# Optimization experiments

Measured on AMD Instinct MI355X. Metric: run time of the kernel, lower is better.

## Reference

```python
import math
import jax, jax.numpy as jnp
import numpy as np

B, T, C = 2, 2048, 1024
H, HKV, HD = 16, 4, 64  # n_head, n_kv_head, head_dim
G = H // HKV            # GQA groups
WS = 1024               # sliding window size
GATE_CH = 32


def setup_inputs() -> dict:
    key = jax.random.key(0)
    ks = jax.random.split(key, 8)
    x = jax.random.normal(ks[0], (B, T, C), dtype=jnp.float32)
    ve = jax.random.normal(ks[1], (B, T, HKV * HD), dtype=jnp.float32)
    # realistic RoPE tables: half head_dim frequencies
    d = HD // 2
    inv_freq = 1.0 / (10000.0 ** (jnp.arange(d, dtype=jnp.float32) / d))
    angles = jnp.arange(T, dtype=jnp.float32)[:, None] * inv_freq[None, :]  # (T, d)
    cos = jnp.cos(angles)[None, :, None, :]  # (1, T, 1, d)
    sin = jnp.sin(angles)[None, :, None, :]
    s = 0.02
    Wq = s * jax.random.normal(ks[2], (C, H * HD), dtype=jnp.float32)
    Wk = s * jax.random.normal(ks[3], (C, HKV * HD), dtype=jnp.float32)
    Wv = s * jax.random.normal(ks[4], (C, HKV * HD), dtype=jnp.float32)
    Wproj = s * jax.random.normal(ks[5], (C, C), dtype=jnp.float32)
    Wg = s * jax.random.normal(ks[6], (GATE_CH, HKV), dtype=jnp.float32)
    return {"x": x, "ve": ve, "cos": cos, "sin": sin,
            "Wq": Wq, "Wk": Wk, "Wv": Wv, "Wproj": Wproj, "Wg": Wg, "ws": WS}


def _rope(u, cos, sin):
    d = u.shape[-1] // 2
    u1, u2 = u[..., :d], u[..., d:]
    return jnp.concatenate([u1 * cos + u2 * sin, -u1 * sin + u2 * cos], axis=-1)


def _rmsnorm(u):
    eps = jnp.finfo(u.dtype).eps
    return u * jax.lax.rsqrt(jnp.mean(u * u, axis=-1, keepdims=True) + eps)


def reference(x, ve, cos, sin, Wq, Wk, Wv, Wproj, Wg, ws):
    b, t, c = x.shape
    q = (x @ Wq).reshape(b, t, H, HD)
    k = (x @ Wk).reshape(b, t, HKV, HD)
    v = (x @ Wv).reshape(b, t, HKV, HD)
    # value-embedding gate: 2*sigmoid over first 32 channels of x
    gate = 2.0 * jax.nn.sigmoid(x[..., :GATE_CH] @ Wg)  # (b, t, HKV)
    v = v + gate[..., None] * ve.reshape(b, t, HKV, HD)
    q = _rmsnorm(_rope(q, cos, sin))
    k = _rmsnorm(_rope(k, cos, sin))
    # GQA: view q as (b, t, HKV, G, HD), contract against shared k/v per kv-head
    qg = q.reshape(b, t, HKV, G, HD)
    scale = 1.0 / math.sqrt(HD)
    scores = jnp.einsum('bqhgd,bkhd->bhgqk', qg, k) * scale  # (b, HKV, G, t, t)
    pos = jnp.arange(t)
    # key j attends iff i - ws + 1 <= j <= i (sliding causal window)
    mask = (pos[None, :] >= pos[:, None] - ws + 1) & (pos[None, :] <= pos[:, None])
    scores = jnp.where(mask[None, None, None], scores, -jnp.inf)
    attn = jax.nn.softmax(scores, axis=-1)
    y = jnp.einsum('bhgqk,bkhd->bqhgd', attn, v).reshape(b, t, H * HD)
    return y @ Wproj
```

## Files before the change

### kernel.cpp

```cpp
#include <hip/hip_runtime.h>
#include <hip/hip_bf16.h>

#define Bq 2
#define Tq 2048
#define Cq 1024
#define Hq 16
#define HKVq 4
#define HDq 64
#define Gq 4
#define WSq 1024
#define GATE_CHq 32

typedef __attribute__((ext_vector_type(8))) short short8;
typedef __attribute__((ext_vector_type(4))) float f32x4;
typedef __attribute__((ext_vector_type(16))) float f32x16;
typedef __attribute__((ext_vector_type(2))) unsigned int u32x2;
typedef unsigned int u32;
typedef unsigned short u16;

#if __has_builtin(__builtin_amdgcn_exp2f)
#define EXP2(x) __builtin_amdgcn_exp2f(x)
#else
#define EXP2(x) exp2f(x)
#endif

__device__ __forceinline__ u16 f2bf(float f) {
  u32 u = __float_as_uint(f);
  u32 r = (u + 0x7FFFu + ((u >> 16) & 1u)) >> 16;
  return (u16)r;
}
__device__ __forceinline__ float bf2f(u16 u) {
  return __uint_as_float(((u32)u) << 16);
}

__device__ __forceinline__ void gl_lds16(const u16* g, u16* l) {
  __builtin_amdgcn_global_load_lds(
      (const u32 __attribute__((address_space(1)))*)g,
      (u32 __attribute__((address_space(3)))*)l, 16, 0, 0);
}

__global__ __launch_bounds__(256) void qkv_gemm_fused(
    const u16* __restrict__ A, const u16* __restrict__ Bt,
    const float* __restrict__ ve, const float* __restrict__ cosp,
    const float* __restrict__ sinp, const float* __restrict__ gatebuf,
    u16* __restrict__ Qb, u16* __restrict__ Kb, u16* __restrict__ Vtb) {
  __shared__ __attribute__((aligned(16))) u16 As[64 * 64];
  __shared__ __attribute__((aligned(16))) u16 Bs[128 * 64];

  const int bx = blockIdx.x;
  const int bm0 = blockIdx.y * 64, bn0 = bx * 128;
  const int tid = threadIdx.x;
  const int w = tid >> 6, lane = tid & 63;
  const int wm = (w >> 1) * 32, wn = (w & 1) * 64;
  const int quad = lane >> 4, l16 = lane & 15;
  const int K = 1024;

  f32x4 acc[2][4];
#pragma unroll
  for (int mt = 0; mt < 2; mt++)
#pragma unroll
    for (int nt = 0; nt < 4; nt++) acc[mt][nt] = (f32x4){0.f, 0.f, 0.f, 0.f};

  int goffA[2], goffB[4];
#pragma unroll
  for (int i = 0; i < 2; i++) {
    int s = i * 256 + tid;
    int m = s >> 3, gp = s & 7;
    goffA[i] = m * K + (gp ^ (m & 7)) * 8;
  }
#pragma unroll
  for (int i = 0; i < 4; i++) {
    int s = i * 256 + tid;
    int m = s >> 3, gp = s & 7;
    goffB[i] = m * K + (gp ^ (m & 7)) * 8;
  }
  const u16* Ab = A + (long)bm0 * K;
  const u16* Bb = Bt + (long)bn0 * K;

  for (int k0 = 0; k0 < K; k0 += 64) {
    __syncthreads();
#pragma unroll
    for (int i = 0; i < 2; i++)
      gl_lds16(Ab + goffA[i] + k0, &As[(i * 256 + w * 64) * 8]);
#pragma unroll
    for (int i = 0; i < 4; i++)
      gl_lds16(Bb + goffB[i] + k0, &Bs[(i * 256 + w * 64) * 8]);
    __syncthreads();

#pragma unroll
    for (int ks = 0; ks < 2; ks++) {
      short8 af[2], bf[4];
#pragma unroll
      for (int mt = 0; mt < 2; mt++) {
        int ml = wm + mt * 16 + l16;
        af[mt] = *(const short8*)&As[ml * 64 + (((ks * 4 + quad) ^ (ml & 7)) * 8)];
      }
#pragma unroll
      for (int nt = 0; nt < 4; nt++) {
        int nl = wn + nt * 16 + l16;
        bf[nt] = *(const short8*)&Bs[nl * 64 + (((ks * 4 + quad) ^ (nl & 7)) * 8)];
      }
#pragma unroll
      for (int mt = 0; mt < 2; mt++)
#pragma unroll
        for (int nt = 0; nt < 4; nt++)
          acc[mt][nt] = __builtin_amdgcn_mfma_f32_16x16x32_bf16(
              af[mt], bf[nt], acc[mt][nt], 0, 0, 0);
    }
  }

  const int b = bm0 >> 11;
  const int tseq0 = (bm0 & 2047) + wm;

  if (bx < 10) {
    u16* Dst;
    if (bx < 8) {
      int hh = bx * 2 + (w & 1);
      int hkv = hh >> 2, g = hh & 3;
      Dst = Qb + ((long)((b * 4 + hkv) * 4 + g) * Tq) * 64;
    } else {
      int kk = (bx - 8) * 2 + (w & 1);
      Dst = Kb + ((long)(b * 4 + kk) * Tq) * 64;
    }
#pragma unroll
    for (int mt = 0; mt < 2; mt++) {
#pragma unroll
      for (int r = 0; r < 4; r++) {
        int t = tseq0 + mt * 16 + quad * 4 + r;
        float c0 = cosp[t * 32 + l16];
        float s0 = sinp[t * 32 + l16];
        float c1 = cosp[t * 32 + 16 + l16];
        float s1 = sinp[t * 32 + 16 + l16];
        float a0 = acc[mt][0][r], a1 = acc[mt][1][r];
        float a2 = acc[mt][2][r], a3 = acc[mt][3][r];
        float rp0 = a0 * c0 + a2 * s0;
        float rp1 = a1 * c1 + a3 * s1;
        float rp2 = a2 * c0 - a0 * s0;
        float rp3 = a3 * c1 - a1 * s1;
        float ss = rp0 * rp0 + rp1 * rp1 + rp2 * rp2 + rp3 * rp3;
        ss += __shfl_xor(ss, 1);
        ss += __shfl_xor(ss, 2);
        ss += __shfl_xor(ss, 4);
        ss += __shfl_xor(ss, 8);
        float sc = rsqrtf(ss * (1.f / 64.f) + 1.1920928955078125e-07f);
        u16* drow = Dst + (long)t * 64;
        drow[l16] = f2bf(rp0 * sc);
        drow[16 + l16] = f2bf(rp1 * sc);
        drow[32 + l16] = f2bf(rp2 * sc);
        drow[48 + l16] = f2bf(rp3 * sc);
      }
    }
  } else {
    int kk = (bx - 10) * 2 + (w & 1);
    u16* Dst = Vtb + ((long)(b * 4 + kk) * 64) * Tq;
#pragma unroll
    for (int mt = 0; mt < 2; mt++) {
      float vals[4][4];
#pragma unroll
      for (int r = 0; r < 4; r++) {
        int t = tseq0 + mt * 16 + quad * 4 + r;
        long bt = (long)b * Tq + t;
        float gv = gatebuf[bt * 4 + kk];
        const float* verow = ve + bt * 256 + kk * 64;
#pragma unroll
        for (int nt = 0; nt < 4; nt++)
          vals[nt][r] = acc[mt][nt][r] + gv * verow[nt * 16 + l16];
      }
      int t0m = tseq0 + mt * 16 + quad * 4;
#pragma unroll
      for (int nt = 0; nt < 4; nt++) {
        int d = nt * 16 + l16;
        union { short4 v; u16 u[4]; } p;
#pragma unroll
        for (int r = 0; r < 4; r++) p.u[r] = f2bf(vals[nt][r]);
        *(short4*)(Dst + (long)d * Tq + t0m) = p.v;
      }
    }
  }
}

__global__ __launch_bounds__(256) void gemm_proj(
    const u16* __restrict__ A, const u16* __restrict__ Bt,
    float* __restrict__ C, int M, int N, int K) {
  __shared__ __attribute__((aligned(16))) u16 As[64 * 64];
  __shared__ __attribute__((aligned(16))) u16 Bs[128 * 64];

  const int bm0 = blockIdx.y * 64, bn0 = blockIdx.x * 128;
  const int tid = threadIdx.x;
  const int w = tid >> 6, lane = tid & 63;
  const int wm = (w >> 1) * 32, wn = (w & 1) * 64;
  const int quad = lane >> 4, l16 = lane & 15;

  f32x4 acc[2][4];
#pragma unroll
  for (int mt = 0; mt < 2; mt++)
#pragma unroll
    for (int nt = 0; nt < 4; nt++) acc[mt][nt] = (f32x4){0.f, 0.f, 0.f, 0.f};

  int goffA[2], goffB[4];
#pragma unroll
  for (int i = 0; i < 2; i++) {
    int s = i * 256 + tid;
    int m = s >> 3, gp = s & 7;
    goffA[i] = m * K + (gp ^ (m & 7)) * 8;
  }
#pragma unroll
  for (int i = 0; i < 4; i++) {
    int s = i * 256 + tid;
    int m = s >> 3, gp = s & 7;
    goffB[i] = m * K + (gp ^ (m & 7)) * 8;
  }
  const u16* Ab = A + (long)bm0 * K;
  const u16* Bb = Bt + (long)bn0 * K;

  for (int k0 = 0; k0 < K; k0 += 64) {
    __syncthreads();
#pragma unroll
    for (int i = 0; i < 2; i++)
      gl_lds16(Ab + goffA[i] + k0, &As[(i * 256 + w * 64) * 8]);
#pragma unroll
    for (int i = 0; i < 4; i++)
      gl_lds16(Bb + goffB[i] + k0, &Bs[(i * 256 + w * 64) * 8]);
    __syncthreads();

#pragma unroll
    for (int ks = 0; ks < 2; ks++) {
      short8 af[2], bf[4];
#pragma unroll
      for (int mt = 0; mt < 2; mt++) {
        int ml = wm + mt * 16 + l16;
        af[mt] = *(const short8*)&As[ml * 64 + (((ks * 4 + quad) ^ (ml & 7)) * 8)];
      }
#pragma unroll
      for (int nt = 0; nt < 4; nt++) {
        int nl = wn + nt * 16 + l16;
        bf[nt] = *(const short8*)&Bs[nl * 64 + (((ks * 4 + quad) ^ (nl & 7)) * 8)];
      }
#pragma unroll
      for (int mt = 0; mt < 2; mt++)
#pragma unroll
        for (int nt = 0; nt < 4; nt++)
          acc[mt][nt] = __builtin_amdgcn_mfma_f32_16x16x32_bf16(
              af[mt], bf[nt], acc[mt][nt], 0, 0, 0);
    }
  }

#pragma unroll
  for (int mt = 0; mt < 2; mt++)
#pragma unroll
    for (int nt = 0; nt < 4; nt++) {
      int row0 = bm0 + wm + mt * 16 + quad * 4;
      int col = bn0 + wn + nt * 16 + l16;
#pragma unroll
      for (int r = 0; r < 4; r++)
        C[(long)(row0 + r) * N + col] = acc[mt][nt][r];
    }
}

__global__ __launch_bounds__(256) void prep(
    const float* __restrict__ x, u16* __restrict__ xb,
    const float* __restrict__ Wq, const float* __restrict__ Wk,
    const float* __restrict__ Wv, const float* __restrict__ Wproj,
    const float* __restrict__ Wg, u16* __restrict__ Dqkv,
    u16* __restrict__ Dproj, float* __restrict__ gatebuf) {
  __shared__ float tile[64][65];
  int bx = blockIdx.x;
  int tid = threadIdx.x;
  if (bx < 2048) {
    int i = (bx * 256 + tid) * 8;
    float4 a = *(const float4*)(x + i);
    float4 b = *(const float4*)(x + i + 4);
    union { short8 v; u16 u[8]; } o;
    o.u[0] = f2bf(a.x); o.u[1] = f2bf(a.y); o.u[2] = f2bf(a.z); o.u[3] = f2bf(a.w);
    o.u[4] = f2bf(b.x); o.u[5] = f2bf(b.y); o.u[6] = f2bf(b.z); o.u[7] = f2bf(b.w);
    *(short8*)(xb + i) = o.v;
    return;
  }
  if (bx >= 2688) {
    int p = (bx - 2688) * 256 + tid;
    int bt = p >> 2, kk = p & 3;
    const float* xr = x + (long)bt * Cq;
    float dot = 0.f;
#pragma unroll
    for (int i = 0; i < GATE_CHq; i++) dot += xr[i] * Wg[i * HKVq + kk];
    gatebuf[p] = 2.f / (1.f + expf(-dot));
    return;
  }
  int wb = bx - 2048;
  int obx = wb >> 4;
  int k0 = (wb & 15) * 64;
  const float* S;
  u16* Dst;
  int N, nb;
  if (obx < 16)      { S = Wq;    N = 1024; nb = obx;      Dst = Dqkv; }
  else if (obx < 20) { S = Wk;    N = 256;  nb = obx - 16; Dst = Dqkv + 1024 * 1024; }
  else if (obx < 24) { S = Wv;    N = 256;  nb = obx - 20; Dst = Dqkv + 1280 * 1024; }
  else               { S = Wproj; N = 1024; nb = obx - 24; Dst = Dproj; }
  int n0 = nb * 64;
#pragma unroll
  for (int i = 0; i < 16; i++) {
    int idx = i * 256 + tid;
    int kl = idx >> 6, nl = idx & 63;
    tile[kl][nl] = S[(long)(k0 + kl) * N + n0 + nl];
  }
  __syncthreads();
#pragma unroll
  for (int i = 0; i < 16; i++) {
    int idx = i * 256 + tid;
    int nl = idx >> 6, kl = idx & 63;
    Dst[(long)(n0 + nl) * 1024 + k0 + kl] = f2bf(tile[kl][nl]);
  }
}

#define CEXP 0.18033688011112042f
#define CEXP8 1.4426950408889634f

template <bool MASK>
__device__ __forceinline__ void attn_tile32(
    int k0, int q0, int l31, int hl, const u16* __restrict__ Ks,
    const u16* __restrict__ Vts, const short8 (&QB)[4], f32x16& O0, f32x16& O1,
    float& lsum) {
  const int qpos = q0 + l31;
#pragma unroll
  for (int c = 0; c < 4; c++) {
    const int key = c * 32 + l31;
    f32x16 S;
#pragma unroll
    for (int i = 0; i < 16; i++) S[i] = 0.f;
#pragma unroll
    for (int s = 0; s < 4; s++) {
      short8 kf = *(const short8*)&Ks[key * 64 + (((s * 2 + hl) ^ (key & 7)) * 8)];
      S = __builtin_amdgcn_mfma_f32_32x32x16_bf16(kf, QB[s], S, 0, 0, 0);
    }
    const int kb = k0 + c * 32 + 4 * hl;
    float p[16];
#pragma unroll
    for (int r = 0; r < 16; r++) {
      float sv = S[r];
      if (MASK) {
        int kpos = kb + (r & 3) + 8 * (r >> 2);
        u32 diff = (u32)(qpos - kpos);
        sv = (diff < (u32)WSq) ? sv : -1e30f;
      }
      float pv = EXP2(__builtin_fmaf(sv, CEXP, -CEXP8));
      lsum += pv;
      p[r] = pv;
    }
    u32 w[8];
#pragma unroll
    for (int i = 0; i < 8; i++) {
      u32 lo = __float_as_uint(p[2 * i]) + 0x8000u;
      u32 hi = __float_as_uint(p[2 * i + 1]) + 0x8000u;
      w[i] = __builtin_amdgcn_perm(hi, lo, 0x07060302u);
    }
    u32x2 r02 = __builtin_amdgcn_permlane32_swap(w[0], w[2], false, false);
    u32x2 r13 = __builtin_amdgcn_permlane32_swap(w[1], w[3], false, false);
    u32x2 r46 = __builtin_amdgcn_permlane32_swap(w[4], w[6], false, false);
    u32x2 r57 = __builtin_amdgcn_permlane32_swap(w[5], w[7], false, false);
    union { short8 s8; u32 u[4]; } f0, f1;
    f0.u[0] = r02[0]; f0.u[1] = r13[0]; f0.u[2] = r02[1]; f0.u[3] = r13[1];
    f1.u[0] = r46[0]; f1.u[1] = r57[0]; f1.u[2] = r46[1]; f1.u[3] = r57[1];
    const int d0 = l31, d1 = 32 + l31;
    const int sw = (l31 & 7);
#pragma unroll
    for (int kc = 0; kc < 2; kc++) {
      int grp = c * 4 + kc * 2 + hl;
      short8 v0 = *(const short8*)&Vts[d0 * 128 + ((grp ^ sw) * 8)];
      short8 v1 = *(const short8*)&Vts[d1 * 128 + ((grp ^ sw) * 8)];
      const short8 pf = kc ? f1.s8 : f0.s8;
      O0 = __builtin_amdgcn_mfma_f32_32x32x16_bf16(v0, pf, O0, 0, 0, 0);
      O1 = __builtin_amdgcn_mfma_f32_32x32x16_bf16(v1, pf, O1, 0, 0, 0);
    }
  }
}

__global__ __launch_bounds__(256, 2) void attn_mfma(
    const u16* __restrict__ Qb, const u16* __restrict__ Kb,
    const u16* __restrict__ Vtb, u16* __restrict__ Yb) {
  __shared__ __attribute__((aligned(16))) u16 Ks[2][128 * 64];
  __shared__ __attribute__((aligned(16))) u16 Vts[2][64 * 128];

  int bid = blockIdx.x;
  int bh = bid & 7;
  int qt32 = bid >> 3;
  int hkv = bh & 3;
  int b = bh >> 2;
  int q0 = qt32 * 32;
  int tid = threadIdx.x;
  int g = tid >> 6;
  int lane = tid & 63;
  int l31 = lane & 31;
  int hl = lane >> 5;

  short8 QB[4];
  {
    const u16* qb =
        Qb + ((long)((bh * 4 + g) * Tq + q0 + l31)) * 64 + hl * 8;
#pragma unroll
    for (int s = 0; s < 4; s++) QB[s] = *(const short8*)(qb + s * 16);
  }

  f32x16 O0, O1;
#pragma unroll
  for (int i = 0; i < 16; i++) { O0[i] = 0.f; O1[i] = 0.f; }
  float lsum = 0.f;

  int lo = q0 - (WSq - 1);
  int st = (lo < 0 ? 0 : lo) >> 7;
  int et = (q0 + 31) >> 7;

  const u16* Kbase = Kb + ((long)bh * Tq) * 64;
  const u16* Vbase = Vtb + ((long)bh * 64) * Tq;

  int rowoffK[4], rowoffV[4];
#pragma unroll
  for (int i = 0; i < 4; i++) {
    int s = i * 256 + tid;
    int kr = s >> 3, kgp = s & 7;
    rowoffK[i] = kr * 64 + (kgp ^ (kr & 7)) * 8;
    int d = s >> 4, vgp = s & 15;
    rowoffV[i] = d * Tq + (vgp ^ (d & 7)) * 8;
  }

  {
    int k0 = st << 7;
#pragma unroll
    for (int i = 0; i < 4; i++) {
      gl_lds16(Kbase + (long)k0 * 64 + rowoffK[i], &Ks[0][(i * 256 + g * 64) * 8]);
      gl_lds16(Vbase + k0 + rowoffV[i], &Vts[0][(i * 256 + g * 64) * 8]);
    }
  }
  __syncthreads();

  int cur = 0;
  for (int kt = st; kt <= et; kt++) {
    int k0 = kt << 7;
    if (kt < et) {
      int k0n = k0 + 128;
#pragma unroll
      for (int i = 0; i < 4; i++) {
        gl_lds16(Kbase + (long)k0n * 64 + rowoffK[i],
                 &Ks[cur ^ 1][(i * 256 + g * 64) * 8]);
        gl_lds16(Vbase + k0n + rowoffV[i],
                 &Vts[cur ^ 1][(i * 256 + g * 64) * 8]);
      }
    }
    bool needC = (k0 + 127 > q0);
    bool needW = (k0 < q0 - 992);
    if (needC || needW) {
      attn_tile32<true>(k0, q0, l31, hl, Ks[cur], Vts[cur], QB, O0, O1, lsum);
    } else {
      attn_tile32<false>(k0, q0, l31, hl, Ks[cur], Vts[cur], QB, O0, O1, lsum);
    }
    __syncthreads();
    cur ^= 1;
  }

  lsum += __shfl_xor(lsum, 32);
  float invl = 1.f / lsum;

  int h = hkv * 4 + g;
  u16* yrow = Yb + ((long)(b * Tq + q0 + l31)) * 1024 + h * 64;
#pragma unroll
  for (int g4 = 0; g4 < 4; g4++) {
    union { short4 v; u16 u[4]; } pk0, pk1;
#pragma unroll
    for (int i = 0; i < 4; i++) {
      pk0.u[i] = f2bf(O0[g4 * 4 + i] * invl);
      pk1.u[i] = f2bf(O1[g4 * 4 + i] * invl);
    }
    int dA = 8 * g4 + 4 * hl;
    *(short4*)(yrow + dA) = pk0.v;
    *(short4*)(yrow + 32 + dA) = pk1.v;
  }
}

extern "C" void kernel_launch(void* const* d_in, const int* in_sizes, int n_in,
                              void* d_out, int out_size, void* d_ws,
                              size_t ws_size, hipStream_t stream) {
  const float* x     = (const float*)d_in[0];
  const float* ve    = (const float*)d_in[1];
  const float* cosp  = (const float*)d_in[2];
  const float* sinp  = (const float*)d_in[3];
  const float* Wq    = (const float*)d_in[4];
  const float* Wk    = (const float*)d_in[5];
  const float* Wv    = (const float*)d_in[6];
  const float* Wproj = (const float*)d_in[7];
  const float* Wg    = (const float*)d_in[8];

  char* base = (char*)d_ws;
  u16* xb      = (u16*)(base);
  u16* Yb      = xb;
  u16* WqkvT   = (u16*)(base + 8388608);
  u16* WprojT  = (u16*)(base + 11534336);
  u16* Qb      = (u16*)(base + 13631488);
  u16* Kb      = (u16*)(base + 22020096);
  u16* Vtb     = (u16*)(base + 24117248);
  float* gateb = (float*)(base + 26214400);
  float* out = (float*)d_out;

  prep<<<2752, 256, 0, stream>>>(x, xb, Wq, Wk, Wv, Wproj, Wg, WqkvT, WprojT,
                                 gateb);
  qkv_gemm_fused<<<dim3(12, 64), 256, 0, stream>>>(xb, WqkvT, ve, cosp, sinp,
                                                   gateb, Qb, Kb, Vtb);
  attn_mfma<<<512, 256, 0, stream>>>(Qb, Kb, Vtb, Yb);
  gemm_proj<<<dim3(8, 64), 256, 0, stream>>>(Yb, WprojT, out, 4096, 1024, 1024);
}
```

Baseline: 162.7 us.

## Enlarge GEMM tiles to 128x128 and add MFMA priority hints in attention

Both the QKV and projection GEMMs now use 128x128 block tiles, with each wave computing a 64x64 sub-tile, so operand reuse per LDS load goes up and the grid halves. The attention inner loop wraps its MFMA sections in s_setprio and splits the softmax row-sum into two accumulators to shorten the dependency chain. The larger tiles raise register and LDS use and leave fewer blocks (384 and 256) to spread across the CUs.

Result: slower. 172.9 us (+6.2%).

```diff
diff --git a/kernel.cpp b/kernel.cpp
--- a/kernel.cpp
+++ b/kernel.cpp
@@ -29,9 +29,6 @@
   u32 r = (u + 0x7FFFu + ((u >> 16) & 1u)) >> 16;
   return (u16)r;
 }
-__device__ __forceinline__ float bf2f(u16 u) {
-  return __uint_as_float(((u32)u) << 16);
-}
 
 __device__ __forceinline__ void gl_lds16(const u16* g, u16* l) {
   __builtin_amdgcn_global_load_lds(
@@ -44,35 +41,29 @@
     const float* __restrict__ ve, const float* __restrict__ cosp,
     const float* __restrict__ sinp, const float* __restrict__ gatebuf,
     u16* __restrict__ Qb, u16* __restrict__ Kb, u16* __restrict__ Vtb) {
-  __shared__ __attribute__((aligned(16))) u16 As[64 * 64];
+  __shared__ __attribute__((aligned(16))) u16 As[128 * 64];
   __shared__ __attribute__((aligned(16))) u16 Bs[128 * 64];
 
   const int bx = blockIdx.x;
-  const int bm0 = blockIdx.y * 64, bn0 = bx * 128;
+  const int bm0 = blockIdx.y * 128, bn0 = bx * 128;
   const int tid = threadIdx.x;
   const int w = tid >> 6, lane = tid & 63;
-  const int wm = (w >> 1) * 32, wn = (w & 1) * 64;
+  const int wm = (w >> 1) * 64, wn = (w & 1) * 64;
   const int quad = lane >> 4, l16 = lane & 15;
   const int K = 1024;
 
-  f32x4 acc[2][4];
-#pragma unroll
-  for (int mt = 0; mt < 2; mt++)
+  f32x4 acc[4][4];
+#pragma unroll
+  for (int mt = 0; mt < 4; mt++)
 #pragma unroll
     for (int nt = 0; nt < 4; nt++) acc[mt][nt] = (f32x4){0.f, 0.f, 0.f, 0.f};
 
-  int goffA[2], goffB[4];
-#pragma unroll
-  for (int i = 0; i < 2; i++) {
-    int s = i * 256 + tid;
-    int m = s >> 3, gp = s & 7;
-    goffA[i] = m * K + (gp ^ (m & 7)) * 8;
-  }
+  int goff[4];
 #pragma unroll
   for (int i = 0; i < 4; i++) {
     int s = i * 256 + tid;
     int m = s >> 3, gp = s & 7;
-    goffB[i] = m * K + (gp ^ (m & 7)) * 8;
+    goff[i] = m * K + (gp ^ (m & 7)) * 8;
   }
   const u16* Ab = A + (long)bm0 * K;
   const u16* Bb = Bt + (long)bn0 * K;
@@ -80,18 +71,17 @@
   for (int k0 = 0; k0 < K; k0 += 64) {
     __syncthreads();
 #pragma unroll
-    for (int i = 0; i < 2; i++)
-      gl_lds16(Ab + goffA[i] + k0, &As[(i * 256 + w * 64) * 8]);
-#pragma unroll
-    for (int i = 0; i < 4; i++)
-      gl_lds16(Bb + goffB[i] + k0, &Bs[(i * 256 + w * 64) * 8]);
+    for (int i = 0; i < 4; i++) {
+      gl_lds16(Ab + goff[i] + k0, &As[(i * 256 + w * 64) * 8]);
+      gl_lds16(Bb + goff[i] + k0, &Bs[(i * 256 + w * 64) * 8]);
+    }
     __syncthreads();
 
 #pragma unroll
     for (int ks = 0; ks < 2; ks++) {
-      short8 af[2], bf[4];
-#pragma unroll
-      for (int mt = 0; mt < 2; mt++) {
+      short8 af[4], bf[4];
+#pragma unroll
+      for (int mt = 0; mt < 4; mt++) {
         int ml = wm + mt * 16 + l16;
         af[mt] = *(const short8*)&As[ml * 64 + (((ks * 4 + quad) ^ (ml & 7)) * 8)];
       }
@@ -101,7 +91,7 @@
         bf[nt] = *(const short8*)&Bs[nl * 64 + (((ks * 4 + quad) ^ (nl & 7)) * 8)];
       }
 #pragma unroll
-      for (int mt = 0; mt < 2; mt++)
+      for (int mt = 0; mt < 4; mt++)
 #pragma unroll
         for (int nt = 0; nt < 4; nt++)
           acc[mt][nt] = __builtin_amdgcn_mfma_f32_16x16x32_bf16(
@@ -123,7 +113,7 @@
       Dst = Kb + ((long)(b * 4 + kk) * Tq) * 64;
     }
 #pragma unroll
-    for (int mt = 0; mt < 2; mt++) {
+    for (int mt = 0; mt < 4; mt++) {
 #pragma unroll
       for (int r = 0; r < 4; r++) {
         int t = tseq0 + mt * 16 + quad * 4 + r;
@@ -154,7 +144,7 @@
     int kk = (bx - 10) * 2 + (w & 1);
     u16* Dst = Vtb + ((long)(b * 4 + kk) * 64) * Tq;
 #pragma unroll
-    for (int mt = 0; mt < 2; mt++) {
+    for (int mt = 0; mt < 4; mt++) {
       float vals[4][4];
 #pragma unroll
       for (int r = 0; r < 4; r++) {
@@ -170,10 +160,10 @@
 #pragma unroll
       for (int nt = 0; nt < 4; nt++) {
         int d = nt * 16 + l16;
-        union { short4 v; u16 u[4]; } p;
-#pragma unroll
-        for (int r = 0; r < 4; r++) p.u[r] = f2bf(vals[nt][r]);
-        *(short4*)(Dst + (long)d * Tq + t0m) = p.v;
+        union { short4 v; u16 u[4]; } pk;
+#pragma unroll
+        for (int r = 0; r < 4; r++) pk.u[r] = f2bf(vals[nt][r]);
+        *(short4*)(Dst + (long)d * Tq + t0m) = pk.v;
       }
     }
   }
@@ -182,33 +172,27 @@
 __global__ __launch_bounds__(256) void gemm_proj(
     const u16* __restrict__ A, const u16* __restrict__ Bt,
     float* __restrict__ C, int M, int N, int K) {
-  __shared__ __attribute__((aligned(16))) u16 As[64 * 64];
+  __shared__ __attribute__((aligned(16))) u16 As[128 * 64];
   __shared__ __attribute__((aligned(16))) u16 Bs[128 * 64];
 
-  const int bm0 = blockIdx.y * 64, bn0 = blockIdx.x * 128;
+  const int bm0 = blockIdx.y * 128, bn0 = blockIdx.x * 128;
   const int tid = threadIdx.x;
   const int w = tid >> 6, lane = tid & 63;
-  const int wm = (w >> 1) * 32, wn = (w & 1) * 64;
+  const int wm = (w >> 1) * 64, wn = (w & 1) * 64;
   const int quad = lane >> 4, l16 = lane & 15;
 
-  f32x4 acc[2][4];
-#pragma unroll
-  for (int mt = 0; mt < 2; mt++)
+  f32x4 acc[4][4];
+#pragma unroll
+  for (int mt = 0; mt < 4; mt++)
 #pragma unroll
     for (int nt = 0; nt < 4; nt++) acc[mt][nt] = (f32x4){0.f, 0.f, 0.f, 0.f};
 
-  int goffA[2], goffB[4];
-#pragma unroll
-  for (int i = 0; i < 2; i++) {
-    int s = i * 256 + tid;
-    int m = s >> 3, gp = s & 7;
-    goffA[i] = m * K + (gp ^ (m & 7)) * 8;
-  }
+  int goff[4];
 #pragma unroll
   for (int i = 0; i < 4; i++) {
     int s = i * 256 + tid;
     int m = s >> 3, gp = s & 7;
-    goffB[i] = m * K + (gp ^ (m & 7)) * 8;
+    goff[i] = m * K + (gp ^ (m & 7)) * 8;
   }
   const u16* Ab = A + (long)bm0 * K;
   const u16* Bb = Bt + (long)bn0 * K;
@@ -216,18 +200,17 @@
   for (int k0 = 0; k0 < K; k0 += 64) {
     __syncthreads();
 #pragma unroll
-    for (int i = 0; i < 2; i++)
-      gl_lds16(Ab + goffA[i] + k0, &As[(i * 256 + w * 64) * 8]);
-#pragma unroll
-    for (int i = 0; i < 4; i++)
-      gl_lds16(Bb + goffB[i] + k0, &Bs[(i * 256 + w * 64) * 8]);
+    for (int i = 0; i < 4; i++) {
+      gl_lds16(Ab + goff[i] + k0, &As[(i * 256 + w * 64) * 8]);
+      gl_lds16(Bb + goff[i] + k0, &Bs[(i * 256 + w * 64) * 8]);
+    }
     __syncthreads();
 
 #pragma unroll
     for (int ks = 0; ks < 2; ks++) {
-      short8 af[2], bf[4];
-#pragma unroll
-      for (int mt = 0; mt < 2; mt++) {
+      short8 af[4], bf[4];
+#pragma unroll
+      for (int mt = 0; mt < 4; mt++) {
         int ml = wm + mt * 16 + l16;
         af[mt] = *(const short8*)&As[ml * 64 + (((ks * 4 + quad) ^ (ml & 7)) * 8)];
       }
@@ -237,7 +220,7 @@
         bf[nt] = *(const short8*)&Bs[nl * 64 + (((ks * 4 + quad) ^ (nl & 7)) * 8)];
       }
 #pragma unroll
-      for (int mt = 0; mt < 2; mt++)
+      for (int mt = 0; mt < 4; mt++)
 #pragma unroll
         for (int nt = 0; nt < 4; nt++)
           acc[mt][nt] = __builtin_amdgcn_mfma_f32_16x16x32_bf16(
@@ -246,7 +229,7 @@
   }
 
 #pragma unroll
-  for (int mt = 0; mt < 2; mt++)
+  for (int mt = 0; mt < 4; mt++)
 #pragma unroll
     for (int nt = 0; nt < 4; nt++) {
       int row0 = bm0 + wm + mt * 16 + quad * 4;
@@ -327,13 +310,16 @@
     f32x16 S;
 #pragma unroll
     for (int i = 0; i < 16; i++) S[i] = 0.f;
+    __builtin_amdgcn_s_setprio(1);
 #pragma unroll
     for (int s = 0; s < 4; s++) {
       short8 kf = *(const short8*)&Ks[key * 64 + (((s * 2 + hl) ^ (key & 7)) * 8)];
       S = __builtin_amdgcn_mfma_f32_32x32x16_bf16(kf, QB[s], S, 0, 0, 0);
     }
+    __builtin_amdgcn_s_setprio(0);
     const int kb = k0 + c * 32 + 4 * hl;
     float p[16];
+    float la0 = 0.f, la1 = 0.f;
 #pragma unroll
     for (int r = 0; r < 16; r++) {
       float sv = S[r];
@@ -343,25 +329,27 @@
         sv = (diff < (u32)WSq) ? sv : -1e30f;
       }
       float pv = EXP2(__builtin_fmaf(sv, CEXP, -CEXP8));
-      lsum += pv;
+      if (r & 1) la1 += pv; else la0 += pv;
       p[r] = pv;
     }
-    u32 w[8];
+    lsum += la0 + la1;
+    u32 w8[8];
 #pragma unroll
     for (int i = 0; i < 8; i++) {
       u32 lo = __float_as_uint(p[2 * i]) + 0x8000u;
       u32 hi = __float_as_uint(p[2 * i + 1]) + 0x8000u;
-      w[i] = __builtin_amdgcn_perm(hi, lo, 0x07060302u);
-    }
-    u32x2 r02 = __builtin_amdgcn_permlane32_swap(w[0], w[2], false, false);
-    u32x2 r13 = __builtin_amdgcn_permlane32_swap(w[1], w[3], false, false);
-    u32x2 r46 = __builtin_amdgcn_permlane32_swap(w[4], w[6], false, false);
-    u32x2 r57 = __builtin_amdgcn_permlane32_swap(w[5], w[7], false, false);
+      w8[i] = __builtin_amdgcn_perm(hi, lo, 0x07060302u);
+    }
+    u32x2 r02 = __builtin_amdgcn_permlane32_swap(w8[0], w8[2], false, false);
+    u32x2 r13 = __builtin_amdgcn_permlane32_swap(w8[1], w8[3], false, false);
+    u32x2 r46 = __builtin_amdgcn_permlane32_swap(w8[4], w8[6], false, false);
+    u32x2 r57 = __builtin_amdgcn_permlane32_swap(w8[5], w8[7], false, false);
     union { short8 s8; u32 u[4]; } f0, f1;
     f0.u[0] = r02[0]; f0.u[1] = r13[0]; f0.u[2] = r02[1]; f0.u[3] = r13[1];
     f1.u[0] = r46[0]; f1.u[1] = r57[0]; f1.u[2] = r46[1]; f1.u[3] = r57[1];
     const int d0 = l31, d1 = 32 + l31;
     const int sw = (l31 & 7);
+    __builtin_amdgcn_s_setprio(1);
 #pragma unroll
     for (int kc = 0; kc < 2; kc++) {
       int grp = c * 4 + kc * 2 + hl;
@@ -371,6 +359,7 @@
       O0 = __builtin_amdgcn_mfma_f32_32x32x16_bf16(v0, pf, O0, 0, 0, 0);
       O1 = __builtin_amdgcn_mfma_f32_32x32x16_bf16(v1, pf, O1, 0, 0, 0);
     }
+    __builtin_amdgcn_s_setprio(0);
   }
 }
 
@@ -497,12 +486,12 @@
   u16* Kb      = (u16*)(base + 22020096);
   u16* Vtb     = (u16*)(base + 24117248);
   float* gateb = (float*)(base + 26214400);
-  float* out = (float*)d_out;
+  float* out   = (float*)d_out;
 
   prep<<<2752, 256, 0, stream>>>(x, xb, Wq, Wk, Wv, Wproj, Wg, WqkvT, WprojT,
                                  gateb);
-  qkv_gemm_fused<<<dim3(12, 64), 256, 0, stream>>>(xb, WqkvT, ve, cosp, sinp,
+  qkv_gemm_fused<<<dim3(12, 32), 256, 0, stream>>>(xb, WqkvT, ve, cosp, sinp,
                                                    gateb, Qb, Kb, Vtb);
   attn_mfma<<<512, 256, 0, stream>>>(Qb, Kb, Vtb, Yb);
-  gemm_proj<<<dim3(8, 64), 256, 0, stream>>>(Yb, WprojT, out, 4096, 1024, 1024);
-}
+  gemm_proj<<<dim3(8, 32), 256, 0, stream>>>(Yb, WprojT, out, 4096, 1024, 1024);
+}
```
